# Kernel optimization log

Measured on AMD Instinct MI355X. Metric: run time of the kernel, lower is better.

## Reference

```python
import jax, jax.numpy as jnp
import numpy as np

N, H, E, K, C, M = 4096, 512, 512, 64, 128, 4  # tokens, hidden, embed, categories, children/cat, max_num_children
IN = E + H  # LSTMCell input size


def setup_inputs() -> dict:
    key = jax.random.key(0)
    ks = jax.random.split(key, 12)
    s = 0.05
    return {
        "et": jax.random.normal(ks[0], (N, H), jnp.float32),
        "x": jax.random.normal(ks[1], (N, IN), jnp.float32),
        "h": jax.random.normal(ks[2], (N, H), jnp.float32),
        "c": jax.random.normal(ks[3], (N, H), jnp.float32),
        "cat": jax.random.randint(ks[4], (N,), 0, K, jnp.int32),
        "ci": jax.random.randint(ks[5], (N,), 0, M, jnp.int32),
        # per-category prediction Linear(hidden_size -> |children(category)|)
        "W_lin": jax.random.normal(ks[6], (K, C, H), jnp.float32) * s,
        "b_lin": jax.random.normal(ks[7], (K, C), jnp.float32) * s,
        # per-child-index LSTMCell(embedding+hidden -> hidden), torch gate order i,f,g,o
        "W_ih": jax.random.normal(ks[8], (M, 4 * H, IN), jnp.float32) * s,
        "W_hh": jax.random.normal(ks[9], (M, 4 * H, H), jnp.float32) * s,
        "b_ih": jax.random.normal(ks[10], (M, 4 * H), jnp.float32) * s,
        "b_hh": jax.random.normal(ks[11], (M, 4 * H), jnp.float32) * s,
    }


def reference(et, x, h, c, cat, ci, W_lin, b_lin, W_ih, W_hh, b_ih, b_hh):
    # get_log_odds: route each token to its category's Linear (gather weights, per-token matvec)
    Wg = W_lin[cat]                                   # [N, C, H]
    log_odds = jnp.einsum('nh,nch->nc', et, Wg) + b_lin[cat]  # [N, C]

    # get_next: LSTMCell selected by child_index. Only M=4 cells, so compute all
    # cells' gates densely (efficient GEMMs) and select with a one-hot mix.
    gates_all = (jnp.einsum('ni,kgi->nkg', x, W_ih)
                 + jnp.einsum('nh,kgh->nkg', h, W_hh)
                 + (b_ih + b_hh)[None])               # [N, M, 4H]
    sel = jax.nn.one_hot(ci, M, dtype=gates_all.dtype)  # [N, M]
    gates = jnp.einsum('nkg,nk->ng', gates_all, sel)     # [N, 4H]
    i_, f_, g_, o_ = jnp.split(gates, 4, axis=-1)
    c2 = jax.nn.sigmoid(f_) * c + jax.nn.sigmoid(i_) * jnp.tanh(g_)
    h2 = jax.nn.sigmoid(o_) * jnp.tanh(c2)
    return log_odds, h2, c2
```

## Files before the change

kernel.cpp:

```cpp
#include <hip/hip_runtime.h>
#include <hip/hip_bf16.h>
#include <stdint.h>

#define NTOK 4096
#define HID  512
#define INSZ 1024
#define KIN  1536
#define KCAT 64
#define CCH  128
#define MCELL 4
#define G4H  2048

typedef unsigned short u16;
typedef __bf16 bf16x8 __attribute__((ext_vector_type(8)));
typedef float  f32x4  __attribute__((ext_vector_type(4)));

__device__ __forceinline__ u16 f2bf(float f) {
    unsigned u = __float_as_uint(f);
    u += 0x7fffu + ((u >> 16) & 1u);
    return (u16)(u >> 16);
}
__device__ __forceinline__ float bf2f(u16 v) {
    return __uint_as_float(((unsigned)v) << 16);
}
__device__ __forceinline__ void store_bf4(u16* p, float4 v) {
    ushort4 r;
    r.x = f2bf(v.x); r.y = f2bf(v.y); r.z = f2bf(v.z); r.w = f2bf(v.w);
    *reinterpret_cast<ushort4*>(p) = r;
}
__device__ __forceinline__ void gl16(const u16* g, u16* l) {
    __builtin_amdgcn_global_load_lds((const __attribute__((address_space(1))) void*)g,
                                     (__attribute__((address_space(3))) void*)l, 16, 0, 0);
}

__global__ __launch_bounds__(1024) void build_perm(
    const int* __restrict__ ci, const int* __restrict__ cat,
    int* __restrict__ meta, int* __restrict__ perm_ci,
    int* __restrict__ inv_ci, int* __restrict__ perm_cat)
{
    __shared__ int cnt_ci[MCELL], cur_ci[MCELL];
    __shared__ int cnt_cat[KCAT], cur_cat[KCAT];
    int tid = threadIdx.x;
    if (tid < MCELL) cnt_ci[tid] = 0;
    if (tid < KCAT)  cnt_cat[tid] = 0;
    __syncthreads();
    for (int t = tid; t < NTOK; t += 1024) {
        atomicAdd(&cnt_ci[ci[t]], 1);
        atomicAdd(&cnt_cat[cat[t]], 1);
    }
    __syncthreads();
    if (tid == 0) {
        int off = 0;
        for (int m = 0; m < MCELL; ++m) {
            int p = (cnt_ci[m] + 127) & ~127;
            meta[m] = p; meta[4 + m] = off; cur_ci[m] = off; off += p;
        }
        off = 0;
        for (int k = 0; k < KCAT; ++k) {
            int p = (cnt_cat[k] + 63) & ~63;
            meta[8 + k] = p; meta[72 + k] = off; cur_cat[k] = off; off += p;
        }
    }
    __syncthreads();
    for (int i = tid; i < 4608; i += 1024) perm_ci[i] = -1;
    for (int i = tid; i < 8192; i += 1024) perm_cat[i] = -1;
    __syncthreads();
    for (int t = tid; t < NTOK; t += 1024) {
        int s = atomicAdd(&cur_ci[ci[t]], 1);
        perm_ci[s] = t; inv_ci[t] = s;
        int sc = atomicAdd(&cur_cat[cat[t]], 1);
        perm_cat[sc] = t;
    }
}

__global__ __launch_bounds__(192) void pack_A(
    const float* __restrict__ x, const float* __restrict__ h,
    const int* __restrict__ perm_ci, u16* __restrict__ A_pack)
{
    int s = blockIdx.x;
    int c = threadIdx.x * 8;
    int t = perm_ci[s];
    u16* dst = A_pack + (size_t)s * KIN + c;
    if (t < 0) {
        *reinterpret_cast<int4*>(dst) = make_int4(0, 0, 0, 0);
        return;
    }
    const float* src = (c < INSZ) ? (x + (size_t)t * INSZ + c)
                                  : (h + (size_t)t * HID + (c - INSZ));
    float4 v0 = *(const float4*)src;
    float4 v1 = *(const float4*)(src + 4);
    store_bf4(dst, v0);
    store_bf4(dst + 4, v1);
}

__global__ __launch_bounds__(192) void pack_W(
    const float* __restrict__ Wih, const float* __restrict__ Whh,
    u16* __restrict__ Wb)
{
    int row = blockIdx.x;
    int m = row >> 11, j = row & 2047;
    int c = threadIdx.x * 8;
    const float* src = (c < INSZ) ? (Wih + ((size_t)m * G4H + j) * INSZ + c)
                                  : (Whh + ((size_t)m * G4H + j) * HID + (c - INSZ));
    u16* dst = Wb + (size_t)row * KIN + c;
    float4 v0 = *(const float4*)src;
    float4 v1 = *(const float4*)(src + 4);
    store_bf4(dst, v0);
    store_bf4(dst + 4, v1);
}

__global__ __launch_bounds__(256, 2) void gates_gemm(
    const u16* __restrict__ A_pack,
    const u16* __restrict__ Wb,
    const int* __restrict__ meta,
    u16* __restrict__ gates)
{
    int rt = blockIdx.x, ct = blockIdx.y, m = blockIdx.z;
    int pcnt = meta[m];
    if (rt * 128 >= pcnt) return;
    int row0 = meta[4 + m] + rt * 128;

    __shared__ __align__(16) u16 As[128 * 32];
    __shared__ __align__(16) u16 Bs[128 * 32];

    int tid = threadIdx.x;
    int lane = tid & 63, wave = tid >> 6;

    int r0 = tid >> 2;
    int cb = tid & 3;
    int kcb = cb ^ ((r0 >> 1) & 3);
    const u16* gA0 = A_pack + (size_t)(row0 + r0) * KIN + kcb * 8;
    const u16* gA1 = gA0 + (size_t)64 * KIN;
    const u16* gB0 = Wb + ((size_t)m * G4H + ct * 128 + r0) * KIN + kcb * 8;
    const u16* gB1 = gB0 + (size_t)64 * KIN;
    u16* lA0 = As + wave * 512;
    u16* lA1 = As + 2048 + wave * 512;
    u16* lB0 = Bs + wave * 512;
    u16* lB1 = Bs + 2048 + wave * 512;

    int wr = wave >> 1, wc = wave & 1;
    int qd = lane >> 4, l15 = lane & 15;
    int qs = (qd ^ ((l15 >> 1) & 3)) * 8;

    f32x4 acc[4][4];
    #pragma unroll
    for (int i = 0; i < 4; ++i)
        #pragma unroll
        for (int j = 0; j < 4; ++j)
            acc[i][j] = (f32x4){0.f, 0.f, 0.f, 0.f};

    for (int ks = 0; ks < KIN / 32; ++ks) {
        gl16(gA0, lA0); gl16(gA1, lA1);
        gl16(gB0, lB0); gl16(gB1, lB1);
        gA0 += 32; gA1 += 32; gB0 += 32; gB1 += 32;
        __syncthreads();

        bf16x8 fa[4], fb[4];
        #pragma unroll
        for (int ti = 0; ti < 4; ++ti)
            fa[ti] = *reinterpret_cast<const bf16x8*>(&As[(wr * 64 + ti * 16 + l15) * 32 + qs]);
        #pragma unroll
        for (int tj = 0; tj < 4; ++tj)
            fb[tj] = *reinterpret_cast<const bf16x8*>(&Bs[(wc * 64 + tj * 16 + l15) * 32 + qs]);
        #pragma unroll
        for (int ti = 0; ti < 4; ++ti)
            #pragma unroll
            for (int tj = 0; tj < 4; ++tj)
                acc[ti][tj] = __builtin_amdgcn_mfma_f32_16x16x32_bf16(fa[ti], fb[tj], acc[ti][tj], 0, 0, 0);
        __syncthreads();
    }

    #pragma unroll
    for (int ti = 0; ti < 4; ++ti) {
        #pragma unroll
        for (int tj = 0; tj < 4; ++tj) {
            int gcol = ct * 128 + wc * 64 + tj * 16 + l15;
            #pragma unroll
            for (int r = 0; r < 4; ++r) {
                int grow = row0 + wr * 64 + ti * 16 + qd * 4 + r;
                gates[(size_t)grow * G4H + gcol] = f2bf(acc[ti][tj][r]);
            }
        }
    }
}

__global__ __launch_bounds__(256) void logodds_gemm(
    const float* __restrict__ et,
    const float* __restrict__ W_lin,
    const float* __restrict__ b_lin,
    const int* __restrict__ meta,
    const int* __restrict__ perm_cat,
    float* __restrict__ out)
{
    int k = blockIdx.x, rt = blockIdx.y;
    int pcnt = meta[8 + k];
    if (rt * 64 >= pcnt) return;
    int base = meta[72 + k] + rt * 64;

    __shared__ int srow[64];
    __shared__ __align__(16) u16 As[64 * 40];
    __shared__ __align__(16) u16 Bs[128 * 40];

    int tid = threadIdx.x;
    if (tid < 64) srow[tid] = perm_cat[base + tid];
    __syncthreads();

    int lane = tid & 63, wave = tid >> 6;
    int qd = lane >> 4, l15 = lane & 15;

    f32x4 acc[4][2];
    #pragma unroll
    for (int i = 0; i < 4; ++i) {
        acc[i][0] = (f32x4){0.f, 0.f, 0.f, 0.f};
        acc[i][1] = (f32x4){0.f, 0.f, 0.f, 0.f};
    }

    const float* Wbase = W_lin + (size_t)k * CCH * HID;

    for (int kk = 0; kk < HID; kk += 32) {
        {
            int r = tid >> 2, cbk = tid & 3;
            u16* dst = &As[r * 40 + cbk * 8];
            int t = srow[r];
            if (t >= 0) {
                const float* s = et + (size_t)t * HID + kk + cbk * 8;
                store_bf4(dst, *(const float4*)s);
                store_bf4(dst + 4, *(const float4*)(s + 4));
            } else {
                *reinterpret_cast<int4*>(dst) = make_int4(0, 0, 0, 0);
            }
        }
        #pragma unroll
        for (int it = 0; it < 2; ++it) {
            int j = it * 256 + tid;
            int r = j >> 2, cbk = j & 3;
            const float* s = Wbase + (size_t)r * HID + kk + cbk * 8;
            u16* dst = &Bs[r * 40 + cbk * 8];
            store_bf4(dst, *(const float4*)s);
            store_bf4(dst + 4, *(const float4*)(s + 4));
        }
        __syncthreads();

        bf16x8 fa[4], fb[2];
        #pragma unroll
        for (int ti = 0; ti < 4; ++ti)
            fa[ti] = *reinterpret_cast<const bf16x8*>(&As[(ti * 16 + l15) * 40 + qd * 8]);
        #pragma unroll
        for (int tj = 0; tj < 2; ++tj)
            fb[tj] = *reinterpret_cast<const bf16x8*>(&Bs[(wave * 32 + tj * 16 + l15) * 40 + qd * 8]);
        #pragma unroll
        for (int ti = 0; ti < 4; ++ti)
            #pragma unroll
            for (int tj = 0; tj < 2; ++tj)
                acc[ti][tj] = __builtin_amdgcn_mfma_f32_16x16x32_bf16(fa[ti], fb[tj], acc[ti][tj], 0, 0, 0);
        __syncthreads();
    }

    #pragma unroll
    for (int ti = 0; ti < 4; ++ti) {
        #pragma unroll
        for (int tj = 0; tj < 2; ++tj) {
            int n = wave * 32 + tj * 16 + l15;
            #pragma unroll
            for (int r = 0; r < 4; ++r) {
                int row = ti * 16 + qd * 4 + r;
                int t = srow[row];
                if (t >= 0)
                    out[(size_t)t * CCH + n] = acc[ti][tj][r] + b_lin[k * CCH + n];
            }
        }
    }
}

__global__ __launch_bounds__(256) void lstm_epilogue(
    const u16* __restrict__ gates,
    const int* __restrict__ meta,
    const int* __restrict__ inv_ci,
    const float* __restrict__ c,
    const float* __restrict__ b_ih,
    const float* __restrict__ b_hh,
    float* __restrict__ out)
{
    int idx = blockIdx.x * 256 + threadIdx.x;
    int t = idx >> 9;
    int hh = idx & 511;
    int s = inv_ci[t];
    int m = (s >= meta[5]) + (s >= meta[6]) + (s >= meta[7]);

    const u16* g = gates + (size_t)s * G4H;
    const float* bi = b_ih + (size_t)m * G4H;
    const float* bh = b_hh + (size_t)m * G4H;
    float gi = bf2f(g[hh])        + bi[hh]        + bh[hh];
    float gf = bf2f(g[512 + hh])  + bi[512 + hh]  + bh[512 + hh];
    float gg = bf2f(g[1024 + hh]) + bi[1024 + hh] + bh[1024 + hh];
    float go = bf2f(g[1536 + hh]) + bi[1536 + hh] + bh[1536 + hh];

    float si = 1.f / (1.f + __expf(-gi));
    float sf = 1.f / (1.f + __expf(-gf));
    float so = 1.f / (1.f + __expf(-go));
    float ct = c[(size_t)t * HID + hh];
    float c2 = sf * ct + si * tanhf(gg);
    float h2 = so * tanhf(c2);

    const size_t o_h2 = (size_t)NTOK * CCH;
    const size_t o_c2 = o_h2 + (size_t)NTOK * HID;
    out[o_h2 + (size_t)t * HID + hh] = h2;
    out[o_c2 + (size_t)t * HID + hh] = c2;
}

extern "C" void kernel_launch(void* const* d_in, const int* in_sizes, int n_in,
                              void* d_out, int out_size, void* d_ws, size_t ws_size,
                              hipStream_t stream) {
    const float* et    = (const float*)d_in[0];
    const float* x     = (const float*)d_in[1];
    const float* h     = (const float*)d_in[2];
    const float* c     = (const float*)d_in[3];
    const int*   cat   = (const int*)d_in[4];
    const int*   ci    = (const int*)d_in[5];
    const float* W_lin = (const float*)d_in[6];
    const float* b_lin = (const float*)d_in[7];
    const float* W_ih  = (const float*)d_in[8];
    const float* W_hh  = (const float*)d_in[9];
    const float* b_ih  = (const float*)d_in[10];
    const float* b_hh  = (const float*)d_in[11];
    float* out = (float*)d_out;

    char* ws = (char*)d_ws;
    int* meta     = (int*)ws;
    int* perm_ci  = (int*)(ws + 1024);
    int* inv_ci   = (int*)(ws + 19456);
    int* perm_cat = (int*)(ws + 35840);
    u16* A_pack   = (u16*)(ws + 68608);
    u16* Wb       = (u16*)(ws + 68608 + 14155776);
    u16* gates    = (u16*)(ws + 68608 + 14155776 + 25165824);

    build_perm<<<1, 1024, 0, stream>>>(ci, cat, meta, perm_ci, inv_ci, perm_cat);
    pack_W<<<MCELL * G4H, 192, 0, stream>>>(W_ih, W_hh, Wb);
    pack_A<<<4608, 192, 0, stream>>>(x, h, perm_ci, A_pack);

    dim3 ggrid(36, 16, MCELL);
    gates_gemm<<<ggrid, 256, 0, stream>>>(A_pack, Wb, meta, gates);

    dim3 lgrid(KCAT, 16);
    logodds_gemm<<<lgrid, 256, 0, stream>>>(et, W_lin, b_lin, meta, perm_cat, out);

    lstm_epilogue<<<(NTOK * HID) / 256, 256, 0, stream>>>(gates, meta, inv_ci, c, b_ih, b_hh, out);
}
```

Before: 274.5 us.

## Merge pack kernels and fuse gates and log-odds GEMMs into one launch

```diff
diff --git a/kernel.cpp b/kernel.cpp
--- a/kernel.cpp
+++ b/kernel.cpp
@@ -73,200 +73,185 @@
     }
 }
 
-__global__ __launch_bounds__(192) void pack_A(
+__global__ __launch_bounds__(192) void pack_all(
     const float* __restrict__ x, const float* __restrict__ h,
-    const int* __restrict__ perm_ci, u16* __restrict__ A_pack)
+    const float* __restrict__ Wih, const float* __restrict__ Whh,
+    const float* __restrict__ W_lin,
+    const int* __restrict__ perm_ci,
+    u16* __restrict__ A_pack, u16* __restrict__ Wb, u16* __restrict__ Wlin)
 {
-    int s = blockIdx.x;
+    int b = blockIdx.x;
     int c = threadIdx.x * 8;
-    int t = perm_ci[s];
-    u16* dst = A_pack + (size_t)s * KIN + c;
-    if (t < 0) {
-        *reinterpret_cast<int4*>(dst) = make_int4(0, 0, 0, 0);
-        return;
-    }
-    const float* src = (c < INSZ) ? (x + (size_t)t * INSZ + c)
-                                  : (h + (size_t)t * HID + (c - INSZ));
-    float4 v0 = *(const float4*)src;
-    float4 v1 = *(const float4*)(src + 4);
-    store_bf4(dst, v0);
-    store_bf4(dst + 4, v1);
-}
-
-__global__ __launch_bounds__(192) void pack_W(
-    const float* __restrict__ Wih, const float* __restrict__ Whh,
-    u16* __restrict__ Wb)
-{
-    int row = blockIdx.x;
-    int m = row >> 11, j = row & 2047;
-    int c = threadIdx.x * 8;
-    const float* src = (c < INSZ) ? (Wih + ((size_t)m * G4H + j) * INSZ + c)
-                                  : (Whh + ((size_t)m * G4H + j) * HID + (c - INSZ));
-    u16* dst = Wb + (size_t)row * KIN + c;
-    float4 v0 = *(const float4*)src;
-    float4 v1 = *(const float4*)(src + 4);
-    store_bf4(dst, v0);
-    store_bf4(dst + 4, v1);
-}
-
-__global__ __launch_bounds__(256, 2) void gates_gemm(
+    if (b < 4608) {
+        int t = perm_ci[b];
+        u16* dst = A_pack + (size_t)b * KIN + c;
+        if (t < 0) {
+            *reinterpret_cast<int4*>(dst) = make_int4(0, 0, 0, 0);
+            return;
+        }
+        const float* src = (c < INSZ) ? (x + (size_t)t * INSZ + c)
+                                      : (h + (size_t)t * HID + (c - INSZ));
+        store_bf4(dst, *(const float4*)src);
+        store_bf4(dst + 4, *(const float4*)(src + 4));
+    } else if (b < 4608 + 8192) {
+        int row = b - 4608;
+        int m = row >> 11, j = row & 2047;
+        const float* src = (c < INSZ) ? (Wih + ((size_t)m * G4H + j) * INSZ + c)
+                                      : (Whh + ((size_t)m * G4H + j) * HID + (c - INSZ));
+        u16* dst = Wb + (size_t)row * KIN + c;
+        store_bf4(dst, *(const float4*)src);
+        store_bf4(dst + 4, *(const float4*)(src + 4));
+    } else {
+        int base = (b - (4608 + 8192)) * 3;
+        int row = base + (c >> 9);
+        int col = c & 511;
+        if (row >= KCAT * CCH) return;
+        const float* src = W_lin + (size_t)row * HID + col;
+        u16* dst = Wlin + (size_t)row * HID + col;
+        store_bf4(dst, *(const float4*)src);
+        store_bf4(dst + 4, *(const float4*)(src + 4));
+    }
+}
+
+__global__ __launch_bounds__(256, 4) void mega_gemm(
     const u16* __restrict__ A_pack,
     const u16* __restrict__ Wb,
-    const int* __restrict__ meta,
-    u16* __restrict__ gates)
-{
-    int rt = blockIdx.x, ct = blockIdx.y, m = blockIdx.z;
-    int pcnt = meta[m];
-    if (rt * 128 >= pcnt) return;
-    int row0 = meta[4 + m] + rt * 128;
-
-    __shared__ __align__(16) u16 As[128 * 32];
-    __shared__ __align__(16) u16 Bs[128 * 32];
-
-    int tid = threadIdx.x;
-    int lane = tid & 63, wave = tid >> 6;
-
-    int r0 = tid >> 2;
-    int cb = tid & 3;
-    int kcb = cb ^ ((r0 >> 1) & 3);
-    const u16* gA0 = A_pack + (size_t)(row0 + r0) * KIN + kcb * 8;
-    const u16* gA1 = gA0 + (size_t)64 * KIN;
-    const u16* gB0 = Wb + ((size_t)m * G4H + ct * 128 + r0) * KIN + kcb * 8;
-    const u16* gB1 = gB0 + (size_t)64 * KIN;
-    u16* lA0 = As + wave * 512;
-    u16* lA1 = As + 2048 + wave * 512;
-    u16* lB0 = Bs + wave * 512;
-    u16* lB1 = Bs + 2048 + wave * 512;
-
-    int wr = wave >> 1, wc = wave & 1;
-    int qd = lane >> 4, l15 = lane & 15;
-    int qs = (qd ^ ((l15 >> 1) & 3)) * 8;
-
-    f32x4 acc[4][4];
-    #pragma unroll
-    for (int i = 0; i < 4; ++i)
-        #pragma unroll
-        for (int j = 0; j < 4; ++j)
-            acc[i][j] = (f32x4){0.f, 0.f, 0.f, 0.f};
-
-    for (int ks = 0; ks < KIN / 32; ++ks) {
-        gl16(gA0, lA0); gl16(gA1, lA1);
-        gl16(gB0, lB0); gl16(gB1, lB1);
-        gA0 += 32; gA1 += 32; gB0 += 32; gB1 += 32;
-        __syncthreads();
-
-        bf16x8 fa[4], fb[4];
-        #pragma unroll
-        for (int ti = 0; ti < 4; ++ti)
-            fa[ti] = *reinterpret_cast<const bf16x8*>(&As[(wr * 64 + ti * 16 + l15) * 32 + qs]);
-        #pragma unroll
-        for (int tj = 0; tj < 4; ++tj)
-            fb[tj] = *reinterpret_cast<const bf16x8*>(&Bs[(wc * 64 + tj * 16 + l15) * 32 + qs]);
-        #pragma unroll
-        for (int ti = 0; ti < 4; ++ti)
-            #pragma unroll
-            for (int tj = 0; tj < 4; ++tj)
-                acc[ti][tj] = __builtin_amdgcn_mfma_f32_16x16x32_bf16(fa[ti], fb[tj], acc[ti][tj], 0, 0, 0);
-        __syncthreads();
-    }
-
-    #pragma unroll
-    for (int ti = 0; ti < 4; ++ti) {
-        #pragma unroll
-        for (int tj = 0; tj < 4; ++tj) {
-            int gcol = ct * 128 + wc * 64 + tj * 16 + l15;
-            #pragma unroll
-            for (int r = 0; r < 4; ++r) {
-                int grow = row0 + wr * 64 + ti * 16 + qd * 4 + r;
-                gates[(size_t)grow * G4H + gcol] = f2bf(acc[ti][tj][r]);
-            }
-        }
-    }
-}
-
-__global__ __launch_bounds__(256) void logodds_gemm(
+    const u16* __restrict__ Wlin,
     const float* __restrict__ et,
-    const float* __restrict__ W_lin,
     const float* __restrict__ b_lin,
     const int* __restrict__ meta,
     const int* __restrict__ perm_cat,
+    u16* __restrict__ gates,
     float* __restrict__ out)
 {
-    int k = blockIdx.x, rt = blockIdx.y;
-    int pcnt = meta[8 + k];
-    if (rt * 64 >= pcnt) return;
-    int base = meta[72 + k] + rt * 64;
-
+    __shared__ __align__(16) u16 As[128 * 32];
+    __shared__ __align__(16) u16 Bs[64 * 32];
     __shared__ int srow[64];
-    __shared__ __align__(16) u16 As[64 * 40];
-    __shared__ __align__(16) u16 Bs[128 * 40];
 
     int tid = threadIdx.x;
-    if (tid < 64) srow[tid] = perm_cat[base + tid];
-    __syncthreads();
-
     int lane = tid & 63, wave = tid >> 6;
+    int r0 = tid >> 2, cb = tid & 3;
+    int kcb = cb ^ ((r0 >> 1) & 3);
     int qd = lane >> 4, l15 = lane & 15;
-
-    f32x4 acc[4][2];
-    #pragma unroll
-    for (int i = 0; i < 4; ++i) {
-        acc[i][0] = (f32x4){0.f, 0.f, 0.f, 0.f};
-        acc[i][1] = (f32x4){0.f, 0.f, 0.f, 0.f};
-    }
-
-    const float* Wbase = W_lin + (size_t)k * CCH * HID;
-
-    for (int kk = 0; kk < HID; kk += 32) {
-        {
-            int r = tid >> 2, cbk = tid & 3;
-            u16* dst = &As[r * 40 + cbk * 8];
-            int t = srow[r];
-            if (t >= 0) {
-                const float* s = et + (size_t)t * HID + kk + cbk * 8;
-                store_bf4(dst, *(const float4*)s);
-                store_bf4(dst + 4, *(const float4*)(s + 4));
+    int qs = (qd ^ ((l15 >> 1) & 3)) * 8;
+
+    if (blockIdx.z < 4) {
+        int m = blockIdx.z, rt = blockIdx.x, ct = blockIdx.y;
+        int pcnt = meta[m];
+        if (rt * 128 >= pcnt) return;
+        int row0 = meta[4 + m] + rt * 128;
+
+        const u16* gA0 = A_pack + (size_t)(row0 + r0) * KIN + kcb * 8;
+        const u16* gA1 = gA0 + (size_t)64 * KIN;
+        const u16* gB0 = Wb + ((size_t)m * G4H + ct * 64 + r0) * KIN + kcb * 8;
+        u16* lA0 = As + wave * 512;
+        u16* lA1 = As + 2048 + wave * 512;
+        u16* lB0 = Bs + wave * 512;
+
+        int wr = wave >> 1, wc = wave & 1;
+
+        f32x4 acc[4][2];
+        #pragma unroll
+        for (int i = 0; i < 4; ++i) {
+            acc[i][0] = (f32x4){0.f, 0.f, 0.f, 0.f};
+            acc[i][1] = (f32x4){0.f, 0.f, 0.f, 0.f};
+        }
+
+        for (int ks = 0; ks < KIN / 32; ++ks) {
+            gl16(gA0, lA0); gl16(gA1, lA1); gl16(gB0, lB0);
+            gA0 += 32; gA1 += 32; gB0 += 32;
+            __syncthreads();
+            bf16x8 fa[4], fb[2];
+            #pragma unroll
+            for (int ti = 0; ti < 4; ++ti)
+                fa[ti] = *reinterpret_cast<const bf16x8*>(&As[(wr * 64 + ti * 16 + l15) * 32 + qs]);
+            #pragma unroll
+            for (int tj = 0; tj < 2; ++tj)
+                fb[tj] = *reinterpret_cast<const bf16x8*>(&Bs[(wc * 32 + tj * 16 + l15) * 32 + qs]);
+            #pragma unroll
+            for (int ti = 0; ti < 4; ++ti)
+                #pragma unroll
+                for (int tj = 0; tj < 2; ++tj)
+                    acc[ti][tj] = __builtin_amdgcn_mfma_f32_16x16x32_bf16(fa[ti], fb[tj], acc[ti][tj], 0, 0, 0);
+            __syncthreads();
+        }
+
+        #pragma unroll
+        for (int ti = 0; ti < 4; ++ti) {
+            #pragma unroll
+            for (int tj = 0; tj < 2; ++tj) {
+                int gcol = ct * 64 + wc * 32 + tj * 16 + l15;
+                #pragma unroll
+                for (int r = 0; r < 4; ++r) {
+                    int grow = row0 + wr * 64 + ti * 16 + qd * 4 + r;
+                    gates[(size_t)grow * G4H + gcol] = f2bf(acc[ti][tj][r]);
+                }
+            }
+        }
+    } else {
+        int id = blockIdx.y * 36 + blockIdx.x;
+        int k = id >> 4, rtl = id & 15;
+        if (k >= KCAT) return;
+        int pcnt = meta[8 + k];
+        if (rtl * 64 >= pcnt) return;
+        int base = meta[72 + k] + rtl * 64;
+
+        if (tid < 64) srow[tid] = perm_cat[base + tid];
+        __syncthreads();
+
+        const u16* gW0 = Wlin + ((size_t)k * CCH + r0) * HID + kcb * 8;
+        const u16* gW1 = gW0 + (size_t)64 * HID;
+        u16* lW0 = As + wave * 512;
+        u16* lW1 = As + 2048 + wave * 512;
+
+        int trow = srow[r0];
+        u16* adst = &Bs[r0 * 32 + (cb ^ ((r0 >> 1) & 3)) * 8];
+        const float* asrc = (trow >= 0) ? (et + (size_t)trow * HID + cb * 8) : nullptr;
+
+        f32x4 acc[4][2];
+        #pragma unroll
+        for (int i = 0; i < 4; ++i) {
+            acc[i][0] = (f32x4){0.f, 0.f, 0.f, 0.f};
+            acc[i][1] = (f32x4){0.f, 0.f, 0.f, 0.f};
+        }
+
+        for (int kk = 0; kk < HID; kk += 32) {
+            gl16(gW0, lW0); gl16(gW1, lW1);
+            gW0 += 32; gW1 += 32;
+            if (asrc) {
+                store_bf4(adst,     *(const float4*)(asrc + kk));
+                store_bf4(adst + 4, *(const float4*)(asrc + kk + 4));
             } else {
-                *reinterpret_cast<int4*>(dst) = make_int4(0, 0, 0, 0);
+                *reinterpret_cast<int4*>(adst) = make_int4(0, 0, 0, 0);
             }
-        }
+            __syncthreads();
+            bf16x8 fa[4], fb[2];
+            #pragma unroll
+            for (int ti = 0; ti < 4; ++ti)
+                fa[ti] = *reinterpret_cast<const bf16x8*>(&Bs[(ti * 16 + l15) * 32 + qs]);
+            #pragma unroll
+            for (int tj = 0; tj < 2; ++tj)
+                fb[tj] = *reinterpret_cast<const bf16x8*>(&As[(wave * 32 + tj * 16 + l15) * 32 + qs]);
+            #pragma unroll
+            for (int ti = 0; ti < 4; ++ti)
+                #pragma unroll
+                for (int tj = 0; tj < 2; ++tj)
+                    acc[ti][tj] = __builtin_amdgcn_mfma_f32_16x16x32_bf16(fa[ti], fb[tj], acc[ti][tj], 0, 0, 0);
+            __syncthreads();
+        }
+
         #pragma unroll
-        for (int it = 0; it < 2; ++it) {
-            int j = it * 256 + tid;
-            int r = j >> 2, cbk = j & 3;
-            const float* s = Wbase + (size_t)r * HID + kk + cbk * 8;
-            u16* dst = &Bs[r * 40 + cbk * 8];
-            store_bf4(dst, *(const float4*)s);
-            store_bf4(dst + 4, *(const float4*)(s + 4));
-        }
-        __syncthreads();
-
-        bf16x8 fa[4], fb[2];
-        #pragma unroll
-        for (int ti = 0; ti < 4; ++ti)
-            fa[ti] = *reinterpret_cast<const bf16x8*>(&As[(ti * 16 + l15) * 40 + qd * 8]);
-        #pragma unroll
-        for (int tj = 0; tj < 2; ++tj)
-            fb[tj] = *reinterpret_cast<const bf16x8*>(&Bs[(wave * 32 + tj * 16 + l15) * 40 + qd * 8]);
-        #pragma unroll
-        for (int ti = 0; ti < 4; ++ti)
-            #pragma unroll
-            for (int tj = 0; tj < 2; ++tj)
-                acc[ti][tj] = __builtin_amdgcn_mfma_f32_16x16x32_bf16(fa[ti], fb[tj], acc[ti][tj], 0, 0, 0);
-        __syncthreads();
-    }
-
-    #pragma unroll
-    for (int ti = 0; ti < 4; ++ti) {
-        #pragma unroll
-        for (int tj = 0; tj < 2; ++tj) {
-            int n = wave * 32 + tj * 16 + l15;
-            #pragma unroll
-            for (int r = 0; r < 4; ++r) {
-                int row = ti * 16 + qd * 4 + r;
-                int t = srow[row];
-                if (t >= 0)
-                    out[(size_t)t * CCH + n] = acc[ti][tj][r] + b_lin[k * CCH + n];
+        for (int ti = 0; ti < 4; ++ti) {
+            #pragma unroll
+            for (int tj = 0; tj < 2; ++tj) {
+                int n = wave * 32 + tj * 16 + l15;
+                #pragma unroll
+                for (int r = 0; r < 4; ++r) {
+                    int row = ti * 16 + qd * 4 + r;
+                    int t = srow[row];
+                    if (t >= 0)
+                        out[(size_t)t * CCH + n] = acc[ti][tj][r] + b_lin[k * CCH + n];
+                }
             }
         }
     }
@@ -332,17 +317,17 @@
     int* perm_cat = (int*)(ws + 35840);
     u16* A_pack   = (u16*)(ws + 68608);
     u16* Wb       = (u16*)(ws + 68608 + 14155776);
-    u16* gates    = (u16*)(ws + 68608 + 14155776 + 25165824);
+    u16* Wlin     = (u16*)(ws + 68608 + 14155776 + 25165824);
+    u16* gates    = (u16*)(ws + 68608 + 14155776 + 25165824 + 8388608);
 
     build_perm<<<1, 1024, 0, stream>>>(ci, cat, meta, perm_ci, inv_ci, perm_cat);
-    pack_W<<<MCELL * G4H, 192, 0, stream>>>(W_ih, W_hh, Wb);
-    pack_A<<<4608, 192, 0, stream>>>(x, h, perm_ci, A_pack);
-
-    dim3 ggrid(36, 16, MCELL);
-    gates_gemm<<<ggrid, 256, 0, stream>>>(A_pack, Wb, meta, gates);
-
-    dim3 lgrid(KCAT, 16);
-    logodds_gemm<<<lgrid, 256, 0, stream>>>(et, W_lin, b_lin, meta, perm_cat, out);
+
+    pack_all<<<4608 + 8192 + 2731, 192, 0, stream>>>(
+        x, h, W_ih, W_hh, W_lin, perm_ci, A_pack, Wb, Wlin);
+
+    dim3 ggrid(36, 32, 5);
+    mega_gemm<<<ggrid, 256, 0, stream>>>(A_pack, Wb, Wlin, et, b_lin, meta,
+                                         perm_cat, gates, out);
 
     lstm_epilogue<<<(NTOK * HID) / 256, 256, 0, stream>>>(gates, meta, inv_ci, c, b_ih, b_hh, out);
 }
```

Result: slower. 281.8 us (+2.7%).
